# Optimization experiments

Hardware: AMD Instinct MI355X
Metric: run time of the kernel (lower is better)

The kernel has to match this reference:

```python
import jax, jax.numpy as jnp
import numpy as np

B, T, C, HS = 1024, 128, 384, 64


def setup_inputs() -> dict:
    key = jax.random.key(0)
    k1, k2, k3, k4 = jax.random.split(key, 4)
    std = 1.0 / np.sqrt(C)  # ~ nn.Linear default init scale
    return {
        "x": jax.random.normal(k1, (B, T, C), dtype=jnp.float32),
        "Wq": jax.random.normal(k2, (C, HS), dtype=jnp.float32) * std,
        "Wk": jax.random.normal(k3, (C, HS), dtype=jnp.float32) * std,
        "Wv": jax.random.normal(k4, (C, HS), dtype=jnp.float32) * std,
    }


def reference(x, Wq, Wk, Wv):
    # x: [B, T, C]; Wq/Wk/Wv: [C, HS]
    q = jnp.einsum("btc,ch->bth", x, Wq)
    k = jnp.einsum("btc,ch->bth", x, Wk)
    v = jnp.einsum("btc,ch->bth", x, Wv)
    scale = 1.0 / jnp.sqrt(jnp.asarray(k.shape[-1], dtype=x.dtype))
    wei = jnp.einsum("bth,bsh->bts", q, k) * scale  # [B, T, T]
    t = x.shape[1]
    causal = jnp.tril(jnp.ones((t, t), dtype=bool))
    wei = jnp.where(causal, wei, jnp.asarray(-jnp.inf, dtype=wei.dtype))
    wei = jax.nn.softmax(wei, axis=-1)
    # dropout omitted (eval mode / deterministic reference)
    out = jnp.einsum("bts,bsh->bth", wei, v)  # [B, T, HS]
    return out
```

## Files before the change

kernel.cpp:

```cpp
#include <hip/hip_runtime.h>


typedef __attribute__((ext_vector_type(8)))  short  short8;
typedef __attribute__((ext_vector_type(16))) float  floatx16;
typedef __attribute__((ext_vector_type(4)))  float  float4v;

#define T_DIM   128
#define C_DIM   384
#define HS      64
#define NCHUNK  12
#define SLAB    1536

#define QK_PITCH 68
#define V_PITCH  132
#define P_PITCH  132
#define Q_OFF 0
#define K_OFF 17408
#define V_OFF 34816
#define LDS_BYTES 51712
#define P_OFF 0
#define XS_OFF 0
#define XS_BUF 16384

#define MFMA(a,b,c) __builtin_amdgcn_mfma_f32_32x32x16_bf16((a),(b),(c),0,0,0)

__device__ inline unsigned short f2bf(float f){
    unsigned u = __builtin_bit_cast(unsigned, f);
    u += 0x7FFFu + ((u >> 16) & 1u);
    return (unsigned short)(u >> 16);
}

__device__ inline short8 ld_b64x2(const char* p){
    union { unsigned long long u[2]; short8 s; } r;
    r.u[0] = *(const unsigned long long*)(p);
    r.u[1] = *(const unsigned long long*)(p + 8);
    return r.s;
}

__global__ void prep_wt(const float* __restrict__ Wq, const float* __restrict__ Wk,
                        const float* __restrict__ Wv, unsigned short* __restrict__ wt){
    int idx = blockIdx.x * 256 + threadIdx.x;
    if (idx >= 48 * SLAB) return;
    int slab = idx / SLAB;
    int rem  = idx - slab * SLAB;
    int n = rem >> 3, j = rem & 7;
    int half = slab & 1, ks = (slab >> 1) & 1, c = slab >> 2;
    int kg = c*32 + ks*16 + half*8 + j;
    const float* W = (n < 64) ? Wq : (n < 128) ? Wk : Wv;
    wt[idx] = f2bf(W[kg * HS + (n & 63)]);
}

__launch_bounds__(256, 3)
__global__ void attn_kernel(const float* __restrict__ x,
                            const unsigned short* __restrict__ wtg,
                            float* __restrict__ out){
    __shared__ __align__(16) char smem[LDS_BYTES];
    const int tid  = threadIdx.x;
    const int lane = tid & 63;
    const int wave = tid >> 6;
    const int l31  = lane & 31;
    const int half = lane >> 5;
    const int koff = half * 8;
    const int b    = blockIdx.x;
    const float* xb = x + (size_t)b * (T_DIM * C_DIM);

    const int mpair = wave & 1;
    const int ntri  = wave >> 1;
    const short8* wf = (const short8*)wtg;
    const int nbase = 96 * ntri + l31;

    const char* xsrc = (const char*)xb
                     + (lane >> 3) * (C_DIM * 4)
                     + ((((lane & 7) ^ (lane >> 3))) << 4);

    auto stage = [&](int c, int sb){
        #pragma unroll
        for (int i = 0; i < 4; ++i){
            const char* g = xsrc + (i*4 + wave) * (8 * C_DIM * 4) + c * 128;
            char*       l = smem + XS_OFF + sb * XS_BUF + (i*4 + wave) * 1024;
            __builtin_amdgcn_global_load_lds(
                (const __attribute__((address_space(1))) unsigned*)g,
                (__attribute__((address_space(3))) unsigned*)l,
                16, 0, 0);
        }
    };

    floatx16 acc[6] = {};
    stage(0, 0);

    #pragma unroll
    for (int c = 0; c < NCHUNK; ++c){
        __syncthreads();

        short8 bfr[2][3];
        #pragma unroll
        for (int ks = 0; ks < 2; ++ks)
            #pragma unroll
            for (int nbl = 0; nbl < 3; ++nbl)
                bfr[ks][nbl] = wf[((c*2 + ks)*2 + half)*192 + nbase + 32*nbl];

        if (c + 1 < NCHUNK) stage(c + 1, (c + 1) & 1);

        const char* sbuf = smem + XS_OFF + (c & 1) * XS_BUF;
        short8 afr[2][2];
        #pragma unroll
        for (int mbl = 0; mbl < 2; ++mbl){
            const int R  = 64*mpair + 32*mbl + l31;
            const char* rp = sbuf + R * 128;
            const int sw = (R & 7) << 4;
            #pragma unroll
            for (int ks = 0; ks < 2; ++ks){
                const int cb = ks*64 + half*32;
                float4v lo = *(const float4v*)(rp + ((cb     ) ^ sw));
                float4v hi = *(const float4v*)(rp + ((cb + 16) ^ sw));
                short8 a;
                a[0]=(short)f2bf(lo[0]); a[1]=(short)f2bf(lo[1]);
                a[2]=(short)f2bf(lo[2]); a[3]=(short)f2bf(lo[3]);
                a[4]=(short)f2bf(hi[0]); a[5]=(short)f2bf(hi[1]);
                a[6]=(short)f2bf(hi[2]); a[7]=(short)f2bf(hi[3]);
                afr[ks][mbl] = a;
            }
        }
        #pragma unroll
        for (int ks = 0; ks < 2; ++ks)
            #pragma unroll
            for (int nbl = 0; nbl < 3; ++nbl){
                acc[nbl*2+0] = MFMA(afr[ks][0], bfr[ks][nbl], acc[nbl*2+0]);
                acc[nbl*2+1] = MFMA(afr[ks][1], bfr[ks][nbl], acc[nbl*2+1]);
            }
    }
    __syncthreads();

    const float QSCALE = 0.125f * 1.44269504088896f;
    #pragma unroll
    for (int nbl = 0; nbl < 3; ++nbl)
        #pragma unroll
        for (int mbl = 0; mbl < 2; ++mbl){
            floatx16 A = acc[nbl*2+mbl];
            int nb = 3*ntri + nbl;
            int mb = 2*mpair + mbl;
            if (nb < 4){
                int base  = (nb < 2) ? Q_OFF : K_OFF;
                int col   = 32 * (nb & 1) + l31;
                float sc  = (nb < 2) ? QSCALE : 1.0f;
                char* bp  = smem + base + col * 2;
                #pragma unroll
                for (int r = 0; r < 16; ++r){
                    int t = 32*mb + (r&3) + 8*(r>>2) + 4*half;
                    *(unsigned short*)(bp + t * (QK_PITCH*2)) = f2bf(A[r] * sc);
                }
            } else {
                int h = 32*(nb-4) + l31;
                char* bp = smem + V_OFF + h * (V_PITCH*2);
                #pragma unroll
                for (int g = 0; g < 4; ++g){
                    int t0 = 32*mb + 8*g + 4*half;
                    union { unsigned short s[4]; unsigned long long u; } pk;
                    pk.s[0]=f2bf(A[4*g+0]); pk.s[1]=f2bf(A[4*g+1]);
                    pk.s[2]=f2bf(A[4*g+2]); pk.s[3]=f2bf(A[4*g+3]);
                    *(unsigned long long*)(bp + t0*2) = pk.u;
                }
            }
        }
    __syncthreads();

    floatx16 accS[4] = {};
    #pragma unroll
    for (int ks = 0; ks < 4; ++ks){
        short8 aq = ld_b64x2(smem + Q_OFF + (32*wave + l31)*(QK_PITCH*2) + (ks*16 + koff)*2);
        #pragma unroll
        for (int st = 0; st < 4; ++st)
            if (st <= wave){
                short8 bk = ld_b64x2(smem + K_OFF + (32*st + l31)*(QK_PITCH*2) + (ks*16 + koff)*2);
                accS[st] = MFMA(aq, bk, accS[st]);
            }
    }
    #pragma unroll
    for (int st = 0; st < 4; ++st)
        if (st <= wave){
            #pragma unroll
            for (int r = 0; r < 16; ++r){
                int trow = (r&3) + 8*(r>>2) + 4*half;
                float e = exp2f(accS[st][r]);
                if (st == wave && l31 > trow) e = 0.0f;
                accS[st][r] = e;
            }
        }

    float linv[16];
    #pragma unroll
    for (int r = 0; r < 16; ++r){
        float l = accS[0][r] + accS[1][r] + accS[2][r] + accS[3][r];
        #pragma unroll
        for (int m = 1; m <= 16; m <<= 1)
            l += __shfl_xor(l, m);
        linv[r] = 1.0f / l;
    }
    __syncthreads();

    #pragma unroll
    for (int st = 0; st < 4; ++st)
        if (st <= wave){
            char* bp = smem + P_OFF + (32*st + l31) * 2;
            #pragma unroll
            for (int r = 0; r < 16; ++r){
                int t = 32*wave + (r&3) + 8*(r>>2) + 4*half;
                *(unsigned short*)(bp + t * (P_PITCH*2)) = f2bf(accS[st][r]);
            }
        }
    __syncthreads();

    floatx16 accO0 = {}, accO1 = {};
    const int nks = 2 * (wave + 1);
    #pragma unroll
    for (int ks = 0; ks < 8; ++ks)
        if (ks < nks){
            short8 ap  = ld_b64x2(smem + P_OFF + (32*wave + l31)*(P_PITCH*2) + (ks*16 + koff)*2);
            short8 bv0 = ld_b64x2(smem + V_OFF + l31        *(V_PITCH*2) + (ks*16 + koff)*2);
            short8 bv1 = ld_b64x2(smem + V_OFF + (l31 + 32) *(V_PITCH*2) + (ks*16 + koff)*2);
            accO0 = MFMA(ap, bv0, accO0);
            accO1 = MFMA(ap, bv1, accO1);
        }

    float* ob = out + (size_t)b * (T_DIM * HS);
    #pragma unroll
    for (int r = 0; r < 16; ++r){
        int t = 32*wave + (r&3) + 8*(r>>2) + 4*half;
        ob[t*HS + l31]      = accO0[r] * linv[r];
        ob[t*HS + l31 + 32] = accO1[r] * linv[r];
    }
}

extern "C" void kernel_launch(void* const* d_in, const int* in_sizes, int n_in,
                              void* d_out, int out_size, void* d_ws, size_t ws_size,
                              hipStream_t stream){
    const float* x  = (const float*)d_in[0];
    const float* Wq = (const float*)d_in[1];
    const float* Wk = (const float*)d_in[2];
    const float* Wv = (const float*)d_in[3];
    unsigned short* wt = (unsigned short*)d_ws;

    prep_wt<<<288, 256, 0, stream>>>(Wq, Wk, Wv, wt);
    attn_kernel<<<1024, 256, 0, stream>>>(x, wt, (float*)d_out);
}
```

Baseline: 311.2 us.

## Triple-buffer x staging and prefetch weight fragments one chunk ahead

The projection loop now uses three LDS buffers for x chunks, issuing async global-to-LDS loads two chunks ahead. The per-iteration __syncthreads is replaced with explicit vmcnt waits plus a raw barrier, so the next chunk's loads can stay in flight while the current chunk is computed. Weight fragments are double-buffered in registers and fetched one chunk early. The launch-bounds occupancy hint drops from 3 to 2 blocks to free registers for the extra buffers, which may reduce latency hiding across blocks.

```diff
diff --git a/kernel.cpp b/kernel.cpp
--- a/kernel.cpp
+++ b/kernel.cpp
@@ -50,7 +50,7 @@
     wt[idx] = f2bf(W[kg * HS + (n & 63)]);
 }
 
-__launch_bounds__(256, 3)
+__launch_bounds__(256, 2)
 __global__ void attn_kernel(const float* __restrict__ x,
                             const unsigned short* __restrict__ wtg,
                             float* __restrict__ out){
@@ -86,22 +86,32 @@
     };
 
     floatx16 acc[6] = {};
+    short8 bfr[2][2][3];
+
+    #pragma unroll
+    for (int ks = 0; ks < 2; ++ks)
+        #pragma unroll
+        for (int nbl = 0; nbl < 3; ++nbl)
+            bfr[0][ks][nbl] = wf[((0*2 + ks)*2 + half)*192 + nbase + 32*nbl];
     stage(0, 0);
+    stage(1, 1);
+    asm volatile("s_waitcnt vmcnt(4)" ::: "memory");
+    __builtin_amdgcn_s_barrier();
+    asm volatile("" ::: "memory");
 
     #pragma unroll
     for (int c = 0; c < NCHUNK; ++c){
-        __syncthreads();
-
-        short8 bfr[2][3];
-        #pragma unroll
-        for (int ks = 0; ks < 2; ++ks)
-            #pragma unroll
-            for (int nbl = 0; nbl < 3; ++nbl)
-                bfr[ks][nbl] = wf[((c*2 + ks)*2 + half)*192 + nbase + 32*nbl];
-
-        if (c + 1 < NCHUNK) stage(c + 1, (c + 1) & 1);
-
-        const char* sbuf = smem + XS_OFF + (c & 1) * XS_BUF;
+        if (c + 1 < NCHUNK){
+            #pragma unroll
+            for (int ks = 0; ks < 2; ++ks)
+                #pragma unroll
+                for (int nbl = 0; nbl < 3; ++nbl)
+                    bfr[(c+1)&1][ks][nbl] =
+                        wf[(((c+1)*2 + ks)*2 + half)*192 + nbase + 32*nbl];
+        }
+        if (c + 2 < NCHUNK) stage(c + 2, (c + 2) % 3);
+
+        const char* sbuf = smem + XS_OFF + (c % 3) * XS_BUF;
         short8 afr[2][2];
         #pragma unroll
         for (int mbl = 0; mbl < 2; ++mbl){
@@ -125,9 +135,16 @@
         for (int ks = 0; ks < 2; ++ks)
             #pragma unroll
             for (int nbl = 0; nbl < 3; ++nbl){
-                acc[nbl*2+0] = MFMA(afr[ks][0], bfr[ks][nbl], acc[nbl*2+0]);
-                acc[nbl*2+1] = MFMA(afr[ks][1], bfr[ks][nbl], acc[nbl*2+1]);
-            }
+                acc[nbl*2+0] = MFMA(afr[ks][0], bfr[c&1][ks][nbl], acc[nbl*2+0]);
+                acc[nbl*2+1] = MFMA(afr[ks][1], bfr[c&1][ks][nbl], acc[nbl*2+1]);
+            }
+
+        if (c + 1 < NCHUNK){
+            if (c < NCHUNK - 2) asm volatile("s_waitcnt vmcnt(10)" ::: "memory");
+            else                asm volatile("s_waitcnt vmcnt(6)"  ::: "memory");
+            __builtin_amdgcn_s_barrier();
+            asm volatile("" ::: "memory");
+        }
     }
     __syncthreads();
 
```

Measured after the change: 304.6 us. 1.02x faster.
